# Optimization experiments

Hardware: AMD Instinct MI355X
Metric: run time of the kernel (lower is better)

Reference implementation:

```python
import jax, jax.numpy as jnp
import numpy as np

B, L, H = 32, 2048, 512


def setup_inputs() -> dict:
    key = jax.random.key(0)
    k1, k2, k3, k4, k5, k6 = jax.random.split(key, 6)
    scale = 1.0 / np.sqrt(H)
    return {
        "query": jax.random.normal(k1, (B, H), dtype=jnp.float32),
        "ref": jax.random.normal(k2, (B, L, H), dtype=jnp.float32),
        "mask": jax.random.randint(k3, (B, L), 0, 2) == 1,
        # learned params (torch Linear weight layout: [out, in]; apply as x @ W.T)
        "W_ref": jax.random.normal(k4, (H, H), dtype=jnp.float32) * scale,
        "W_q": jax.random.normal(k5, (H, H), dtype=jnp.float32) * scale,
        "v": jax.random.normal(k6, (H,), dtype=jnp.float32) * scale,
    }


def reference(query, ref, mask, W_ref, W_q, v):
    scale = 1.0 / np.sqrt(H)
    # additive (Bahdanau) scores: v^T tanh(W_ref ref + W_q q)
    encoded_ref = jnp.einsum("blh,oh->blo", ref, W_ref)          # (B, L, H)
    encoded_q = jnp.einsum("bh,oh->bo", query, W_q)[:, None, :]  # (B, 1, H)
    scores = jnp.einsum("blh,h->bl", jnp.tanh(encoded_ref + encoded_q), v)
    scores = scores * scale
    scores = jnp.where(mask, -1e9, scores)
    attn = jax.nn.softmax(scores, axis=1)                         # (B, L)
    glimpse = jnp.einsum("bl,blh->bh", attn, ref)                 # (B, H)
    return glimpse, scores
```

## Files before the change

### kernel.cpp

```cpp
#include <hip/hip_runtime.h>
#include <hip/hip_bf16.h>
#include <cstdint>

typedef __attribute__((ext_vector_type(4))) float f32x4;
typedef __attribute__((ext_vector_type(8))) short s16x8;

#define NB   32
#define NL   2048
#define NH   512
#define NM   (NB * NL)
#define SCALE 0.04419417382415922f

__device__ __forceinline__ ushort f2bf(float f) {
    __hip_bfloat16 b = __float2bfloat16(f);
    return *reinterpret_cast<ushort*>(&b);
}
__device__ __forceinline__ unsigned long long pack4(float4 f) {
    union { ushort u[4]; unsigned long long v; } p;
    p.u[0] = f2bf(f.x); p.u[1] = f2bf(f.y); p.u[2] = f2bf(f.z); p.u[3] = f2bf(f.w);
    return p.v;
}

#define GL16(g, l)                                                         \
    __builtin_amdgcn_global_load_lds(                                      \
        (const __attribute__((address_space(1))) unsigned int*)(g),        \
        (__attribute__((address_space(3))) unsigned int*)(l), 16, 0, 0)

__global__ __launch_bounds__(256) void k_pre(const float* __restrict__ W,
                                             ushort* __restrict__ Wb,
                                             const float* __restrict__ query,
                                             const float* __restrict__ Wq,
                                             float* __restrict__ eq) {
    int bid = blockIdx.x;
    int t = threadIdx.x;
    if (bid < 64) {
        const float4* F = (const float4*)W;
        unsigned long long* U = (unsigned long long*)Wb;
        int base = bid * 1024 + t;
        float4 f[4];
#pragma unroll
        for (int k = 0; k < 4; ++k) f[k] = F[base + k * 256];
#pragma unroll
        for (int k = 0; k < 4; ++k) U[base + k * 256] = pack4(f[k]);
    } else {
        __shared__ float q[NH];
        int b = bid - 64;
        q[t] = query[b * NH + t];
        q[t + 256] = query[b * NH + t + 256];
        __syncthreads();
#pragma unroll
        for (int half = 0; half < 2; ++half) {
            int o = t + half * 256;
            const float4* w = (const float4*)(Wq + (size_t)o * NH);
            float acc = 0.f;
#pragma unroll 4
            for (int i = 0; i < NH / 4; ++i) {
                float4 x = w[i];
                acc += q[4 * i] * x.x + q[4 * i + 1] * x.y + q[4 * i + 2] * x.z + q[4 * i + 3] * x.w;
            }
            eq[b * NH + o] = acc;
        }
    }
}

__global__ __launch_bounds__(256, 2) void k_gemm_full(const float* __restrict__ ref,
                                                      const ushort* __restrict__ Wb,
                                                      const float* __restrict__ eq,
                                                      const float* __restrict__ v,
                                                      const int* __restrict__ mask,
                                                      float* __restrict__ out_sc) {
    __shared__ char smem[73728];
    ushort* Bs0 = (ushort*)smem;
    ushort* Bs1 = (ushort*)(smem + 32768);
    ushort* As0 = (ushort*)(smem + 65536);
    ushort* As1 = (ushort*)(smem + 69632);

    int tid = threadIdx.x;
    int lane = tid & 63, wid = tid >> 6;
    int blk = blockIdx.x;
    int m0g = blk << 6;
    int b = blk >> 5;

    f32x4 acc[4][8];
#pragma unroll
    for (int i = 0; i < 4; ++i)
#pragma unroll
        for (int j = 0; j < 8; ++j) acc[i][j] = (f32x4)(0.f);

    const ushort* bglob = Wb + ((size_t)(wid * 128) + (lane >> 2)) * NH
                             + ((((lane & 3) ^ ((lane >> 2) & 3))) << 3);
    int arow = tid >> 2, acl = tid & 3;
    const float* aglob = ref + (size_t)(m0g + arow) * NH + acl * 8;
    int awr = arow * 32 + ((acl ^ (arow & 3)) << 3);

    int lr = lane & 15, kq = lane >> 4;
    int bbase = (wid * 128 + lr) * 32 + ((kq ^ (lr & 3)) << 3);
    int abase = lr * 32 + ((kq ^ (lr & 3)) << 3);

    float4 qa0, qa1;

#define LOAD_A(kt)                                              \
    {   qa0 = *(const float4*)(aglob + (kt) * 32);              \
        qa1 = *(const float4*)(aglob + (kt) * 32 + 4); }

#define WRITE_A(Asb)                                            \
    {   union { ushort u[8]; s16x8 v; } p;                      \
        p.u[0] = f2bf(qa0.x); p.u[1] = f2bf(qa0.y);             \
        p.u[2] = f2bf(qa0.z); p.u[3] = f2bf(qa0.w);             \
        p.u[4] = f2bf(qa1.x); p.u[5] = f2bf(qa1.y);             \
        p.u[6] = f2bf(qa1.z); p.u[7] = f2bf(qa1.w);             \
        *(s16x8*)&(Asb)[awr] = p.v; }

#define STAGE_B(Bsb, kt)                                        \
    {   _Pragma("unroll")                                       \
        for (int j = 0; j < 8; ++j)                             \
            GL16(bglob + (kt) * 32 + j * 16 * NH,               \
                 (Bsb) + (wid * 128 + j * 16) * 32); }

#define READ_FRAGS(Bsb, Asb)                                                     \
    _Pragma("unroll")                                                            \
    for (int f = 0; f < 4; ++f) af[f] = *(const s16x8*)&(Asb)[abase + f * 512];  \
    _Pragma("unroll")                                                            \
    for (int f = 0; f < 8; ++f) bfr[f] = *(const s16x8*)&(Bsb)[bbase + f * 512];

#define MFMA_ALL()                                                               \
    __builtin_amdgcn_s_setprio(1);                                               \
    _Pragma("unroll")                                                            \
    for (int fr = 0; fr < 4; ++fr)                                               \
        _Pragma("unroll")                                                        \
        for (int fc = 0; fc < 8; ++fc)                                           \
            acc[fr][fc] = __builtin_amdgcn_mfma_f32_16x16x32_bf16(               \
                af[fr], bfr[fc], acc[fr][fc], 0, 0, 0);                          \
    __builtin_amdgcn_s_setprio(0);

    LOAD_A(0)
    float4 ra0 = qa0, ra1 = qa1;
    LOAD_A(1)
    STAGE_B(Bs0, 0)
    STAGE_B(Bs1, 1)
    asm volatile("s_waitcnt vmcnt(18)" ::: "memory");
    {
        union { ushort u[8]; s16x8 v; } p;
        p.u[0] = f2bf(ra0.x); p.u[1] = f2bf(ra0.y);
        p.u[2] = f2bf(ra0.z); p.u[3] = f2bf(ra0.w);
        p.u[4] = f2bf(ra1.x); p.u[5] = f2bf(ra1.y);
        p.u[6] = f2bf(ra1.z); p.u[7] = f2bf(ra1.w);
        *(s16x8*)&As0[awr] = p.v;
    }
    asm volatile("s_waitcnt lgkmcnt(0)" ::: "memory");
    __builtin_amdgcn_s_barrier();

#pragma unroll 1
    for (int t2 = 0; t2 < 7; ++t2) {
        {
            s16x8 bfr[8], af[4];
            asm volatile("s_waitcnt vmcnt(8)" ::: "memory");
            __builtin_amdgcn_s_barrier();
            READ_FRAGS(Bs0, As0)
            WRITE_A(As1)
            asm volatile("s_waitcnt lgkmcnt(0)" ::: "memory");
            __builtin_amdgcn_sched_barrier(0);
            __builtin_amdgcn_s_barrier();
            LOAD_A(2 * t2 + 2)
            STAGE_B(Bs0, 2 * t2 + 2)
            MFMA_ALL()
        }
        {
            s16x8 bfr[8], af[4];
            asm volatile("s_waitcnt vmcnt(8)" ::: "memory");
            __builtin_amdgcn_s_barrier();
            READ_FRAGS(Bs1, As1)
            WRITE_A(As0)
            asm volatile("s_waitcnt lgkmcnt(0)" ::: "memory");
            __builtin_amdgcn_sched_barrier(0);
            __builtin_amdgcn_s_barrier();
            LOAD_A(2 * t2 + 3)
            STAGE_B(Bs1, 2 * t2 + 3)
            MFMA_ALL()
        }
    }
    {
        s16x8 bfr[8], af[4];
        asm volatile("s_waitcnt vmcnt(8)" ::: "memory");
        __builtin_amdgcn_s_barrier();
        READ_FRAGS(Bs0, As0)
        WRITE_A(As1)
        asm volatile("s_waitcnt lgkmcnt(0)" ::: "memory");
        __builtin_amdgcn_sched_barrier(0);
        __builtin_amdgcn_s_barrier();
        MFMA_ALL()
    }
    {
        s16x8 bfr[8], af[4];
        asm volatile("s_waitcnt vmcnt(0)" ::: "memory");
        __builtin_amdgcn_s_barrier();
        READ_FRAGS(Bs1, As1)
        MFMA_ALL()
    }
#undef LOAD_A
#undef WRITE_A
#undef STAGE_B
#undef READ_FRAGS
#undef MFMA_ALL

    __syncthreads();

    float* sc_red = (float*)smem;
    const float* eqb = eq + b * NH;
    float vv[8], ee[8];
#pragma unroll
    for (int fc = 0; fc < 8; ++fc) {
        int c = wid * 128 + fc * 16 + lr;
        vv[fc] = v[c];
        ee[fc] = eqb[c];
    }
#pragma unroll
    for (int fr = 0; fr < 4; ++fr) {
#pragma unroll
        for (int reg = 0; reg < 4; ++reg) {
            float s = 0.f;
#pragma unroll
            for (int fc = 0; fc < 8; ++fc) {
                float x = acc[fr][fc][reg] + ee[fc];
                float t = 1.f - 2.f / (__expf(2.f * x) + 1.f);
                s += vv[fc] * t;
            }
            s += __shfl_xor(s, 1);
            s += __shfl_xor(s, 2);
            s += __shfl_xor(s, 4);
            s += __shfl_xor(s, 8);
            if (lr == 0) sc_red[wid * 64 + fr * 16 + kq * 4 + reg] = s;
        }
    }
    __syncthreads();
    if (tid < 64) {
        float t = 0.f;
#pragma unroll
        for (int w = 0; w < 4; ++w) t += sc_red[w * 64 + tid];
        t *= SCALE;
        int rg = m0g + tid;
        if (mask[rg] != 0) t = -1e9f;
        out_sc[rg] = t;
    }
}

__global__ __launch_bounds__(256) void k_smglp(const float* __restrict__ scores,
                                               const float* __restrict__ ref,
                                               float* __restrict__ glp) {
    int sp = blockIdx.x, b = blockIdx.y;
    int tid = threadIdx.x;
    int lane = tid & 63, wid = tid >> 6;
    __shared__ float red[4];
    __shared__ float asl[128];
    float sc[8];
    float mx = -3.4e38f;
#pragma unroll
    for (int i = 0; i < 8; ++i) {
        sc[i] = scores[b * NL + i * 256 + tid];
        mx = fmaxf(mx, sc[i]);
    }
#pragma unroll
    for (int o = 32; o >= 1; o >>= 1) mx = fmaxf(mx, __shfl_xor(mx, o));
    if (lane == 0) red[wid] = mx;
    __syncthreads();
    mx = fmaxf(fmaxf(red[0], red[1]), fmaxf(red[2], red[3]));
    __syncthreads();
    float ls = 0.f;
#pragma unroll
    for (int i = 0; i < 8; ++i) {
        float e = __expf(sc[i] - mx);
        ls += e;
        if (i == (sp >> 1) && (tid >> 7) == (sp & 1)) asl[tid & 127] = e;
    }
#pragma unroll
    for (int o = 32; o >= 1; o >>= 1) ls += __shfl_xor(ls, o);
    if (lane == 0) red[wid] = ls;
    __syncthreads();
    float inv = 1.f / (red[0] + red[1] + red[2] + red[3]);

    const float* rb = ref + ((size_t)b * NL + sp * 128) * NH;
    float2 acc = make_float2(0.f, 0.f);
#pragma unroll 4
    for (int l = 0; l < 128; ++l) {
        float a = asl[l];
        float2 r = ((const float2*)(rb + (size_t)l * NH))[tid];
        acc.x += a * r.x;
        acc.y += a * r.y;
    }
    acc.x *= inv;
    acc.y *= inv;
    ((float2*)(glp + (size_t)(sp * NB + b) * NH))[tid] = acc;
}

__global__ __launch_bounds__(256) void k_gred(const float* __restrict__ glp,
                                              float* __restrict__ out_gl) {
    int idx = blockIdx.x * 256 + threadIdx.x;
    float s = 0.f;
#pragma unroll
    for (int sp = 0; sp < 16; ++sp) s += glp[sp * (NB * NH) + idx];
    out_gl[idx] = s;
}

extern "C" void kernel_launch(void* const* d_in, const int* in_sizes, int n_in,
                              void* d_out, int out_size, void* d_ws, size_t ws_size,
                              hipStream_t stream) {
    const float* query = (const float*)d_in[0];
    const float* ref   = (const float*)d_in[1];
    const int*   mask  = (const int*)d_in[2];
    const float* W_ref = (const float*)d_in[3];
    const float* W_q   = (const float*)d_in[4];
    const float* v     = (const float*)d_in[5];

    float* out_gl = (float*)d_out;
    float* out_sc = out_gl + NB * NH;

    char* w = (char*)d_ws;
    ushort* wW = (ushort*)w;
    float* eq  = (float*)(w + 524288);
    float* glp = (float*)(w + 589824);

    k_pre<<<96, 256, 0, stream>>>(W_ref, wW, query, W_q, eq);
    k_gemm_full<<<1024, 256, 0, stream>>>(ref, wW, eq, v, mask, out_sc);
    k_smglp<<<dim3(16, NB), 256, 0, stream>>>(out_sc, ref, glp);
    k_gred<<<64, 256, 0, stream>>>(glp, out_gl);
}
```

Measured before the change: 128.4 us.

## Split GEMM over output columns into two halves with partial score reduction

The fused GEMM+score kernel now computes half of the output columns per block (64x256 tiles instead of 64x512). It doubles the grid, halves shared memory and accumulators so four blocks fit per CU, and remaps blocks across XCDs. Partial scores from the two column halves go to a workspace, and the softmax kernel sums them, applies scale and mask, and writes the scores output. The A-tile load/write pipeline is also reordered. In exchange, every ref tile is read and converted twice, adding global traffic and an extra partial-score round trip.

```diff
diff --git a/kernel.cpp b/kernel.cpp
--- a/kernel.cpp
+++ b/kernel.cpp
@@ -63,38 +63,39 @@
     }
 }
 
-__global__ __launch_bounds__(256, 2) void k_gemm_full(const float* __restrict__ ref,
-                                                      const ushort* __restrict__ Wb,
-                                                      const float* __restrict__ eq,
-                                                      const float* __restrict__ v,
-                                                      const int* __restrict__ mask,
-                                                      float* __restrict__ out_sc) {
-    __shared__ char smem[73728];
+__global__ __launch_bounds__(256, 4) void k_gemm(const float* __restrict__ ref,
+                                                 const ushort* __restrict__ Wb,
+                                                 const float* __restrict__ eq,
+                                                 const float* __restrict__ v,
+                                                 float* __restrict__ part) {
+    __shared__ char smem[40960];
     ushort* Bs0 = (ushort*)smem;
-    ushort* Bs1 = (ushort*)(smem + 32768);
-    ushort* As0 = (ushort*)(smem + 65536);
-    ushort* As1 = (ushort*)(smem + 69632);
+    ushort* Bs1 = (ushort*)(smem + 16384);
+    ushort* As0 = (ushort*)(smem + 32768);
+    ushort* As1 = (ushort*)(smem + 36864);
 
     int tid = threadIdx.x;
     int lane = tid & 63, wid = tid >> 6;
-    int blk = blockIdx.x;
-    int m0g = blk << 6;
-    int b = blk >> 5;
-
-    f32x4 acc[4][8];
+    int phys = blockIdx.x;
+    int xcd = phys & 7, slot = phys >> 3;
+    int mt = xcd * 128 + (slot >> 1);
+    int nt = slot & 1;
+    int m0g = mt * 64, n0 = nt * 256;
+    int b = mt >> 5;
+
+    f32x4 acc[4][4];
 #pragma unroll
     for (int i = 0; i < 4; ++i)
 #pragma unroll
-        for (int j = 0; j < 8; ++j) acc[i][j] = (f32x4)(0.f);
-
-    const ushort* bglob = Wb + ((size_t)(wid * 128) + (lane >> 2)) * NH
-                             + ((((lane & 3) ^ ((lane >> 2) & 3))) << 3);
-    int arow = tid >> 2, acl = tid & 3;
-    const float* aglob = ref + (size_t)(m0g + arow) * NH + acl * 8;
-    int awr = arow * 32 + ((acl ^ (arow & 3)) << 3);
+        for (int j = 0; j < 4; ++j) acc[i][j] = (f32x4)(0.f);
+
+    const ushort* bglob = Wb + ((size_t)(n0 + wid * 64) + (lane >> 2)) * NH
+                             + (((lane & 3) ^ ((lane >> 2) & 3)) << 3);
+    const float* aglob = ref + (size_t)(m0g + (tid >> 2)) * NH + (tid & 3) * 8;
+    int awr = (tid >> 2) * 32 + (((tid & 3) ^ ((tid >> 2) & 3)) << 3);
 
     int lr = lane & 15, kq = lane >> 4;
-    int bbase = (wid * 128 + lr) * 32 + ((kq ^ (lr & 3)) << 3);
+    int bbase = (wid * 64 + lr) * 32 + ((kq ^ (lr & 3)) << 3);
     int abase = lr * 32 + ((kq ^ (lr & 3)) << 3);
 
     float4 qa0, qa1;
@@ -113,88 +114,95 @@
 
 #define STAGE_B(Bsb, kt)                                        \
     {   _Pragma("unroll")                                       \
-        for (int j = 0; j < 8; ++j)                             \
+        for (int j = 0; j < 4; ++j)                             \
             GL16(bglob + (kt) * 32 + j * 16 * NH,               \
-                 (Bsb) + (wid * 128 + j * 16) * 32); }
+                 (Bsb) + (wid * 64 + j * 16) * 32); }
 
 #define READ_FRAGS(Bsb, Asb)                                                     \
     _Pragma("unroll")                                                            \
     for (int f = 0; f < 4; ++f) af[f] = *(const s16x8*)&(Asb)[abase + f * 512];  \
     _Pragma("unroll")                                                            \
-    for (int f = 0; f < 8; ++f) bfr[f] = *(const s16x8*)&(Bsb)[bbase + f * 512];
+    for (int f = 0; f < 4; ++f) bfr[f] = *(const s16x8*)&(Bsb)[bbase + f * 512];
 
 #define MFMA_ALL()                                                               \
     __builtin_amdgcn_s_setprio(1);                                               \
     _Pragma("unroll")                                                            \
     for (int fr = 0; fr < 4; ++fr)                                               \
         _Pragma("unroll")                                                        \
-        for (int fc = 0; fc < 8; ++fc)                                           \
+        for (int fc = 0; fc < 4; ++fc)                                           \
             acc[fr][fc] = __builtin_amdgcn_mfma_f32_16x16x32_bf16(               \
                 af[fr], bfr[fc], acc[fr][fc], 0, 0, 0);                          \
     __builtin_amdgcn_s_setprio(0);
 
-    LOAD_A(0)
-    float4 ra0 = qa0, ra1 = qa1;
-    LOAD_A(1)
-    STAGE_B(Bs0, 0)
-    STAGE_B(Bs1, 1)
-    asm volatile("s_waitcnt vmcnt(18)" ::: "memory");
     {
-        union { ushort u[8]; s16x8 v; } p;
-        p.u[0] = f2bf(ra0.x); p.u[1] = f2bf(ra0.y);
-        p.u[2] = f2bf(ra0.z); p.u[3] = f2bf(ra0.w);
-        p.u[4] = f2bf(ra1.x); p.u[5] = f2bf(ra1.y);
-        p.u[6] = f2bf(ra1.z); p.u[7] = f2bf(ra1.w);
-        *(s16x8*)&As0[awr] = p.v;
-    }
-    asm volatile("s_waitcnt lgkmcnt(0)" ::: "memory");
-    __builtin_amdgcn_s_barrier();
+        float4 ra0 = *(const float4*)(aglob);
+        float4 ra1 = *(const float4*)(aglob + 4);
+        LOAD_A(1)
+        STAGE_B(Bs0, 0)
+        STAGE_B(Bs1, 1)
+        asm volatile("s_waitcnt vmcnt(10)" ::: "memory");
+        {
+            union { ushort u[8]; s16x8 v; } p;
+            p.u[0] = f2bf(ra0.x); p.u[1] = f2bf(ra0.y);
+            p.u[2] = f2bf(ra0.z); p.u[3] = f2bf(ra0.w);
+            p.u[4] = f2bf(ra1.x); p.u[5] = f2bf(ra1.y);
+            p.u[6] = f2bf(ra1.z); p.u[7] = f2bf(ra1.w);
+            *(s16x8*)&As0[awr] = p.v;
+        }
+        asm volatile("s_waitcnt vmcnt(8)" ::: "memory");
+        WRITE_A(As1)
+        asm volatile("s_waitcnt vmcnt(4)" ::: "memory");
+        asm volatile("s_waitcnt lgkmcnt(0)" ::: "memory");
+    }
 
 #pragma unroll 1
     for (int t2 = 0; t2 < 7; ++t2) {
         {
-            s16x8 bfr[8], af[4];
-            asm volatile("s_waitcnt vmcnt(8)" ::: "memory");
+            s16x8 bfr[4], af[4];
+            LOAD_A(2 * t2 + 2)
+            asm volatile("s_waitcnt lgkmcnt(0)" ::: "memory");
             __builtin_amdgcn_s_barrier();
             READ_FRAGS(Bs0, As0)
-            WRITE_A(As1)
             asm volatile("s_waitcnt lgkmcnt(0)" ::: "memory");
             __builtin_amdgcn_sched_barrier(0);
             __builtin_amdgcn_s_barrier();
-            LOAD_A(2 * t2 + 2)
             STAGE_B(Bs0, 2 * t2 + 2)
+            asm volatile("s_waitcnt vmcnt(4)" ::: "memory");
+            WRITE_A(As0)
             MFMA_ALL()
         }
         {
-            s16x8 bfr[8], af[4];
-            asm volatile("s_waitcnt vmcnt(8)" ::: "memory");
+            s16x8 bfr[4], af[4];
+            LOAD_A(2 * t2 + 3)
+            asm volatile("s_waitcnt lgkmcnt(0)" ::: "memory");
             __builtin_amdgcn_s_barrier();
             READ_FRAGS(Bs1, As1)
-            WRITE_A(As0)
             asm volatile("s_waitcnt lgkmcnt(0)" ::: "memory");
             __builtin_amdgcn_sched_barrier(0);
             __builtin_amdgcn_s_barrier();
-            LOAD_A(2 * t2 + 3)
             STAGE_B(Bs1, 2 * t2 + 3)
+            asm volatile("s_waitcnt vmcnt(4)" ::: "memory");
+            WRITE_A(As1)
             MFMA_ALL()
         }
     }
     {
-        s16x8 bfr[8], af[4];
-        asm volatile("s_waitcnt vmcnt(8)" ::: "memory");
+        s16x8 bfr[4], af[4];
+        asm volatile("s_waitcnt lgkmcnt(0)" ::: "memory");
         __builtin_amdgcn_s_barrier();
         READ_FRAGS(Bs0, As0)
-        WRITE_A(As1)
         asm volatile("s_waitcnt lgkmcnt(0)" ::: "memory");
         __builtin_amdgcn_sched_barrier(0);
         __builtin_amdgcn_s_barrier();
+        asm volatile("s_waitcnt vmcnt(0)" ::: "memory");
         MFMA_ALL()
     }
     {
-        s16x8 bfr[8], af[4];
-        asm volatile("s_waitcnt vmcnt(0)" ::: "memory");
+        s16x8 bfr[4], af[4];
+        asm volatile("s_waitcnt lgkmcnt(0)" ::: "memory");
         __builtin_amdgcn_s_barrier();
         READ_FRAGS(Bs1, As1)
+        asm volatile("s_waitcnt lgkmcnt(0)" ::: "memory");
         MFMA_ALL()
     }
 #undef LOAD_A
@@ -207,10 +215,10 @@
 
     float* sc_red = (float*)smem;
     const float* eqb = eq + b * NH;
-    float vv[8], ee[8];
-#pragma unroll
-    for (int fc = 0; fc < 8; ++fc) {
-        int c = wid * 128 + fc * 16 + lr;
+    float vv[4], ee[4];
+#pragma unroll
+    for (int fc = 0; fc < 4; ++fc) {
+        int c = n0 + wid * 64 + fc * 16 + lr;
         vv[fc] = v[c];
         ee[fc] = eqb[c];
     }
@@ -220,7 +228,7 @@
         for (int reg = 0; reg < 4; ++reg) {
             float s = 0.f;
 #pragma unroll
-            for (int fc = 0; fc < 8; ++fc) {
+            for (int fc = 0; fc < 4; ++fc) {
                 float x = acc[fr][fc][reg] + ee[fc];
                 float t = 1.f - 2.f / (__expf(2.f * x) + 1.f);
                 s += vv[fc] * t;
@@ -237,15 +245,14 @@
         float t = 0.f;
 #pragma unroll
         for (int w = 0; w < 4; ++w) t += sc_red[w * 64 + tid];
-        t *= SCALE;
-        int rg = m0g + tid;
-        if (mask[rg] != 0) t = -1e9f;
-        out_sc[rg] = t;
-    }
-}
-
-__global__ __launch_bounds__(256) void k_smglp(const float* __restrict__ scores,
+        part[(size_t)nt * NM + m0g + tid] = t;
+    }
+}
+
+__global__ __launch_bounds__(256) void k_smglp(const float* __restrict__ part,
+                                               const int* __restrict__ mask,
                                                const float* __restrict__ ref,
+                                               float* __restrict__ out_sc,
                                                float* __restrict__ glp) {
     int sp = blockIdx.x, b = blockIdx.y;
     int tid = threadIdx.x;
@@ -256,8 +263,12 @@
     float mx = -3.4e38f;
 #pragma unroll
     for (int i = 0; i < 8; ++i) {
-        sc[i] = scores[b * NL + i * 256 + tid];
-        mx = fmaxf(mx, sc[i]);
+        int m = b * NL + i * 256 + tid;
+        float s = (part[m] + part[NM + m]) * SCALE;
+        if (mask[m] != 0) s = -1e9f;
+        if (sp == 0) out_sc[m] = s;
+        sc[i] = s;
+        mx = fmaxf(mx, s);
     }
 #pragma unroll
     for (int o = 32; o >= 1; o >>= 1) mx = fmaxf(mx, __shfl_xor(mx, o));
@@ -315,12 +326,13 @@
     float* out_sc = out_gl + NB * NH;
 
     char* w = (char*)d_ws;
-    ushort* wW = (ushort*)w;
-    float* eq  = (float*)(w + 524288);
-    float* glp = (float*)(w + 589824);
+    ushort* wW  = (ushort*)w;
+    float* eq   = (float*)(w + 524288);
+    float* part = (float*)(w + 589824);
+    float* glp  = (float*)(w + 1114112);
 
     k_pre<<<96, 256, 0, stream>>>(W_ref, wW, query, W_q, eq);
-    k_gemm_full<<<1024, 256, 0, stream>>>(ref, wW, eq, v, mask, out_sc);
-    k_smglp<<<dim3(16, NB), 256, 0, stream>>>(out_sc, ref, glp);
+    k_gemm<<<2048, 256, 0, stream>>>(ref, wW, eq, v, part);
+    k_smglp<<<dim3(16, NB), 256, 0, stream>>>(part, mask, ref, out_sc, glp);
     k_gred<<<64, 256, 0, stream>>>(glp, out_gl);
 }
```

After: 136.7 us. +6.5%, slower.
